# Kernel optimization log

Measured on AMD Instinct MI355X. Metric: run time of the kernel, lower is better.

## Reference

```python
import jax, jax.numpy as jnp
import numpy as np

N, E = 50000, 800000
IN_DIM, OUT_DIM, REL_DIM = 128, 64, 32
NEG_SLOPE = 0.01  # torch F.leaky_relu default


def setup_inputs() -> dict:
    key = jax.random.key(0)
    ks = jax.random.split(key, 12)
    return {
        "h": jax.random.normal(ks[0], (N, IN_DIM), jnp.float32),
        "relation": jax.random.normal(ks[1], (E, REL_DIM), jnp.float32),
        "score": jax.random.normal(ks[2], (E, 1), jnp.float32),
        "timestamp": jax.random.normal(ks[3], (E, 1), jnp.float32),
        "src": jax.random.randint(ks[4], (E,), 0, N, jnp.int32),
        "dst": jax.random.randint(ks[5], (E,), 0, N, jnp.int32),
        "W_n": jax.random.normal(ks[6], (IN_DIM, OUT_DIM), jnp.float32) / np.sqrt(IN_DIM),
        "W_r": jax.random.normal(ks[7], (REL_DIM, OUT_DIM), jnp.float32) / np.sqrt(REL_DIM),
        "W_s": jax.random.normal(ks[8], (1, OUT_DIM), jnp.float32),
        "W_t": jax.random.normal(ks[9], (1, OUT_DIM), jnp.float32),
        "a": jax.random.normal(ks[10], (5 * OUT_DIM,), jnp.float32) / np.sqrt(5 * OUT_DIM),
    }


def reference(h, relation, score, timestamp, src, dst, W_n, W_r, W_s, W_t, a):
    D = W_n.shape[1]
    z = h @ W_n                     # (N, D)
    er = relation @ W_r             # (E, D)
    es = score @ W_s                # (E, D)
    et = timestamp @ W_t            # (E, D)
    z_src = z[src]                  # (E, D) gather
    z_dst = z[dst]                  # (E, D) gather
    # attn_fc on concat([z_src, z_dst, er, es, et]) == sum of slice dot-products
    a1, a2, a3, a4, a5 = (a[0:D], a[D:2*D], a[2*D:3*D], a[3*D:4*D], a[4*D:5*D])
    logit = z_src @ a1 + z_dst @ a2 + er @ a3 + es @ a4 + et @ a5  # (E,)
    logit = jnp.where(logit >= 0, logit, NEG_SLOPE * logit)        # leaky_relu
    # segment softmax over edges grouped by dst node
    n = z.shape[0]
    seg_max = jax.ops.segment_max(logit, dst, num_segments=n)     # (N,)
    ex = jnp.exp(logit - seg_max[dst])                             # (E,)
    seg_sum = jax.ops.segment_sum(ex, dst, num_segments=n)        # (N,)
    alpha = ex / seg_sum[dst]                                      # (E,)
    # weighted scatter-sum of source features to dst nodes
    h_out = jax.ops.segment_sum(alpha[:, None] * z_src, dst, num_segments=n)  # (N, D)
    return h_out
```

## Files before the change

kernel.cpp:

```cpp
#include <hip/hip_runtime.h>

#define IN_DIM 128
#define OUT_DIM 64
#define REL_DIM 32
#define NEG_SLOPE 0.01f
#define CAP 64

__global__ __launch_bounds__(256) void k_node(const float* __restrict__ h,
                                              const float* __restrict__ W_n,
                                              const float* __restrict__ a,
                                              float* __restrict__ z,
                                              float* __restrict__ s1,
                                              float* __restrict__ s2,
                                              int* __restrict__ cnt, int n) {
    __shared__ float hs[IN_DIM * 65];
    __shared__ float Wl[64 * OUT_DIM];
    __shared__ float s1p[4][64], s2p[4][64];
    int base = blockIdx.x * 64;

    int gi = blockIdx.x * 256 + threadIdx.x;
    if (gi < n) cnt[gi] = 0;

    for (int i = threadIdx.x; i < 64 * 32; i += 256) {
        int r = i >> 5;
        int c4 = i & 31;
        float4 v = make_float4(0.f, 0.f, 0.f, 0.f);
        if (base + r < n) v = ((const float4*)(h + (size_t)(base + r) * IN_DIM))[c4];
        int k0 = c4 * 4;
        hs[(k0 + 0) * 65 + r] = v.x;
        hs[(k0 + 1) * 65 + r] = v.y;
        hs[(k0 + 2) * 65 + r] = v.z;
        hs[(k0 + 3) * 65 + r] = v.w;
    }

    int lane = threadIdx.x & 63;
    int w = __builtin_amdgcn_readfirstlane(threadIdx.x >> 6);
    int c0 = w * 16;
    int row = base + lane;

    float acc[16];
    #pragma unroll
    for (int j = 0; j < 16; ++j) acc[j] = 0.f;

    for (int kh = 0; kh < 2; ++kh) {
        __syncthreads();
        for (int i = threadIdx.x; i < 64 * OUT_DIM / 4; i += 256)
            ((float4*)Wl)[i] = ((const float4*)(W_n + (size_t)kh * 64 * OUT_DIM))[i];
        __syncthreads();
        #pragma unroll 4
        for (int kk = 0; kk < 64; ++kk) {
            float hv = hs[(kh * 64 + kk) * 65 + lane];
            const float4* Wk = (const float4*)(Wl + kk * OUT_DIM + c0);
            float4 w0 = Wk[0], w1 = Wk[1], w2 = Wk[2], w3 = Wk[3];
            acc[0]  = fmaf(hv, w0.x, acc[0]);
            acc[1]  = fmaf(hv, w0.y, acc[1]);
            acc[2]  = fmaf(hv, w0.z, acc[2]);
            acc[3]  = fmaf(hv, w0.w, acc[3]);
            acc[4]  = fmaf(hv, w1.x, acc[4]);
            acc[5]  = fmaf(hv, w1.y, acc[5]);
            acc[6]  = fmaf(hv, w1.z, acc[6]);
            acc[7]  = fmaf(hv, w1.w, acc[7]);
            acc[8]  = fmaf(hv, w2.x, acc[8]);
            acc[9]  = fmaf(hv, w2.y, acc[9]);
            acc[10] = fmaf(hv, w2.z, acc[10]);
            acc[11] = fmaf(hv, w2.w, acc[11]);
            acc[12] = fmaf(hv, w3.x, acc[12]);
            acc[13] = fmaf(hv, w3.y, acc[13]);
            acc[14] = fmaf(hv, w3.z, acc[14]);
            acc[15] = fmaf(hv, w3.w, acc[15]);
        }
    }

    float p1 = 0.f, p2 = 0.f;
    #pragma unroll
    for (int j = 0; j < 16; ++j) {
        p1 = fmaf(acc[j], a[c0 + j], p1);
        p2 = fmaf(acc[j], a[OUT_DIM + c0 + j], p2);
    }
    s1p[w][lane] = p1;
    s2p[w][lane] = p2;

    if (row < n) {
        float4* zp = (float4*)(z + (size_t)row * OUT_DIM + c0);
        zp[0] = make_float4(acc[0], acc[1], acc[2], acc[3]);
        zp[1] = make_float4(acc[4], acc[5], acc[6], acc[7]);
        zp[2] = make_float4(acc[8], acc[9], acc[10], acc[11]);
        zp[3] = make_float4(acc[12], acc[13], acc[14], acc[15]);
    }
    __syncthreads();
    if (threadIdx.x < 64 && base + (int)threadIdx.x < n) {
        int l = threadIdx.x;
        s1[base + l] = s1p[0][l] + s1p[1][l] + s1p[2][l] + s1p[3][l];
        s2[base + l] = s2p[0][l] + s2p[1][l] + s2p[2][l] + s2p[3][l];
    }
}

__global__ __launch_bounds__(256) void k_fill(const float* __restrict__ rel,
                                              const float* __restrict__ score,
                                              const float* __restrict__ ts,
                                              const int* __restrict__ src,
                                              const int* __restrict__ dst,
                                              const float* __restrict__ s1,
                                              const float* __restrict__ s2,
                                              const float* __restrict__ W_r,
                                              const float* __restrict__ W_s,
                                              const float* __restrict__ W_t,
                                              const float* __restrict__ a,
                                              int* __restrict__ cnt,
                                              int2* __restrict__ pedge, int E) {
    __shared__ __align__(16) float cw[36];
    int t = threadIdx.x;
    if (t < REL_DIM) {
        const float* a3 = a + 2 * OUT_DIM;
        float acc = 0.f;
        #pragma unroll
        for (int d2 = 0; d2 < OUT_DIM; ++d2)
            acc = fmaf(W_r[t * OUT_DIM + d2], a3[d2], acc);
        cw[t] = acc;
    } else if (t == 32) {
        float acc = 0.f;
        for (int d2 = 0; d2 < OUT_DIM; ++d2) acc = fmaf(W_s[d2], a[3 * OUT_DIM + d2], acc);
        cw[32] = acc;
    } else if (t == 33) {
        float acc = 0.f;
        for (int d2 = 0; d2 < OUT_DIM; ++d2) acc = fmaf(W_t[d2], a[4 * OUT_DIM + d2], acc);
        cw[33] = acc;
    }
    __syncthreads();

    int tid = blockIdx.x * 256 + t;
    int e = tid >> 3;
    int sub = tid & 7;
    if (e >= E) return;

    float4 w4 = ((const float4*)cw)[sub];
    float4 v = ((const float4*)rel)[(size_t)e * 8 + sub];
    float dot = v.x * w4.x + v.y * w4.y + v.z * w4.z + v.w * w4.w;
    dot += __shfl_xor(dot, 1, 8);
    dot += __shfl_xor(dot, 2, 8);
    dot += __shfl_xor(dot, 4, 8);

    if (sub == 0) {
        int s = src[e], d = dst[e];
        float lg = dot + s1[s] + s2[d] + score[e] * cw[32] + ts[e] * cw[33];
        lg = (lg >= 0.f) ? lg : NEG_SLOPE * lg;
        int rank = atomicAdd(cnt + d, 1);
        if (rank < CAP)
            pedge[((size_t)d << 6) + rank] = make_int2(s, __float_as_int(lg));
    }
}

__global__ __launch_bounds__(256) void k_out(const int* __restrict__ cnt,
                                             const int2* __restrict__ pedge,
                                             const float* __restrict__ z,
                                             float* __restrict__ out, int n) {
    int lane = threadIdx.x & 63;
    int wave = (blockIdx.x * blockDim.x + threadIdx.x) >> 6;
    int nwaves = (gridDim.x * blockDim.x) >> 6;
    int eg = lane >> 4;
    int dl = lane & 15;
    int npairs = (n + 1) >> 1;
    for (int p = wave; p < npairs; p += nwaves) {
        int nA = p * 2, nB = p * 2 + 1;
        int degA = min(cnt[nA], CAP);
        int degB = (nB < n) ? min(cnt[nB], CAP) : 0;
        int2 peA = make_int2(0, (int)0xff800000u);
        int2 peB = make_int2(0, (int)0xff800000u);
        if (lane < degA) peA = pedge[((size_t)nA << 6) + lane];
        if (lane < degB) peB = pedge[((size_t)nB << 6) + lane];
        float vA = __int_as_float(peA.y), vB = __int_as_float(peB.y);
        float mA = vA, mB = vB;
        #pragma unroll
        for (int o = 32; o > 0; o >>= 1) {
            mA = fmaxf(mA, __shfl_xor(mA, o, 64));
            mB = fmaxf(mB, __shfl_xor(mB, o, 64));
        }
        float exA = __expf(vA - mA);
        float exB = __expf(vB - mB);
        float sA = exA, sB = exB;
        #pragma unroll
        for (int o = 32; o > 0; o >>= 1) {
            sA += __shfl_xor(sA, o, 64);
            sB += __shfl_xor(sB, o, 64);
        }
        float alA = exA * (1.0f / sA);
        float alB = exB * (1.0f / sB);
        float4 accA = make_float4(0.f, 0.f, 0.f, 0.f);
        float4 accB = make_float4(0.f, 0.f, 0.f, 0.f);
        int jmax = max(degA, degB);
        for (int j0 = 0; j0 < jmax; j0 += 4) {
            int j = j0 + eg;
            int jc = (j < 64) ? j : 63;
            float wA = __shfl(alA, jc, 64);
            int  sjA = __shfl(peA.x, jc, 64);
            float wB = __shfl(alB, jc, 64);
            int  sjB = __shfl(peB.x, jc, 64);
            if (j < degA) {
                float4 zv = ((const float4*)(z + (size_t)sjA * OUT_DIM))[dl];
                accA.x = fmaf(wA, zv.x, accA.x);
                accA.y = fmaf(wA, zv.y, accA.y);
                accA.z = fmaf(wA, zv.z, accA.z);
                accA.w = fmaf(wA, zv.w, accA.w);
            }
            if (j < degB) {
                float4 zv = ((const float4*)(z + (size_t)sjB * OUT_DIM))[dl];
                accB.x = fmaf(wB, zv.x, accB.x);
                accB.y = fmaf(wB, zv.y, accB.y);
                accB.z = fmaf(wB, zv.z, accB.z);
                accB.w = fmaf(wB, zv.w, accB.w);
            }
        }
        #pragma unroll
        for (int o = 16; o <= 32; o <<= 1) {
            accA.x += __shfl_xor(accA.x, o, 64);
            accA.y += __shfl_xor(accA.y, o, 64);
            accA.z += __shfl_xor(accA.z, o, 64);
            accA.w += __shfl_xor(accA.w, o, 64);
            accB.x += __shfl_xor(accB.x, o, 64);
            accB.y += __shfl_xor(accB.y, o, 64);
            accB.z += __shfl_xor(accB.z, o, 64);
            accB.w += __shfl_xor(accB.w, o, 64);
        }
        if (eg == 0) {
            ((float4*)(out + (size_t)nA * OUT_DIM))[dl] = accA;
        } else if (eg == 1 && nB < n) {
            ((float4*)(out + (size_t)nB * OUT_DIM))[dl] = accB;
        }
    }
}

extern "C" void kernel_launch(void* const* d_in, const int* in_sizes, int n_in,
                              void* d_out, int out_size, void* d_ws, size_t ws_size,
                              hipStream_t stream) {
    const float* h         = (const float*)d_in[0];
    const float* relation  = (const float*)d_in[1];
    const float* score     = (const float*)d_in[2];
    const float* timestamp = (const float*)d_in[3];
    const int*   src       = (const int*)d_in[4];
    const int*   dst       = (const int*)d_in[5];
    const float* W_n       = (const float*)d_in[6];
    const float* W_r       = (const float*)d_in[7];
    const float* W_s       = (const float*)d_in[8];
    const float* W_t       = (const float*)d_in[9];
    const float* a         = (const float*)d_in[10];

    int n = in_sizes[0] / IN_DIM;
    int E = in_sizes[4];

    float* ws   = (float*)d_ws;
    float* z    = ws;
    float* s1   = z + (size_t)n * OUT_DIM;
    float* s2   = s1 + n;
    int*   cnt  = (int*)(s2 + n);
    int2*  pedge = (int2*)(cnt + n);

    float* out = (float*)d_out;

    k_node<<<(n + 63) / 64, 256, 0, stream>>>(h, W_n, a, z, s1, s2, cnt, n);

    int nfb = (int)(((long long)E * 8 + 255) / 256);
    k_fill<<<nfb, 256, 0, stream>>>(relation, score, timestamp, src, dst,
                                    s1, s2, W_r, W_s, W_t, a, cnt, pedge, E);

    int npairs = (n + 1) >> 1;
    k_out<<<(npairs + 3) / 4, 256, 0, stream>>>(cnt, pedge, z, out, n);
}
```

Measured before the change: 312.6 us.

## Store node features in fp16 and bucket edge indices instead of packed pairs

Node projections z are written as fp16 so the per-edge gather in the aggregation kernel moves half the bytes, converting back to fp32 before accumulation. The attention constant vector is computed once in the node kernel instead of in every fill block. The per-destination bucket now stores edge ids, with logits written to a separate array, so the output kernel performs extra indirect loads of logit and src. This trades precision of z and additional random 4-byte gathers for lower gather bandwidth.

```diff
diff --git a/kernel.cpp b/kernel.cpp
--- a/kernel.cpp
+++ b/kernel.cpp
@@ -1,4 +1,5 @@
 #include <hip/hip_runtime.h>
+#include <hip/hip_fp16.h>
 
 #define IN_DIM 128
 #define OUT_DIM 64
@@ -8,10 +9,14 @@
 
 __global__ __launch_bounds__(256) void k_node(const float* __restrict__ h,
                                               const float* __restrict__ W_n,
+                                              const float* __restrict__ W_r,
+                                              const float* __restrict__ W_s,
+                                              const float* __restrict__ W_t,
                                               const float* __restrict__ a,
-                                              float* __restrict__ z,
+                                              __half* __restrict__ zh,
                                               float* __restrict__ s1,
                                               float* __restrict__ s2,
+                                              float* __restrict__ consts,
                                               int* __restrict__ cnt, int n) {
     __shared__ float hs[IN_DIM * 65];
     __shared__ float Wl[64 * OUT_DIM];
@@ -20,6 +25,28 @@
 
     int gi = blockIdx.x * 256 + threadIdx.x;
     if (gi < n) cnt[gi] = 0;
+
+    if (blockIdx.x == 0) {
+        int t = threadIdx.x;
+        if (t < REL_DIM) {
+            const float* a3 = a + 2 * OUT_DIM;
+            float acc = 0.f;
+            #pragma unroll
+            for (int d2 = 0; d2 < OUT_DIM; ++d2)
+                acc = fmaf(W_r[t * OUT_DIM + d2], a3[d2], acc);
+            consts[t] = acc;
+        } else if (t == 32) {
+            float acc = 0.f;
+            for (int d2 = 0; d2 < OUT_DIM; ++d2) acc = fmaf(W_s[d2], a[3 * OUT_DIM + d2], acc);
+            consts[32] = acc;
+        } else if (t == 33) {
+            float acc = 0.f;
+            for (int d2 = 0; d2 < OUT_DIM; ++d2) acc = fmaf(W_t[d2], a[4 * OUT_DIM + d2], acc);
+            consts[33] = acc;
+        } else if (t == 34 || t == 35) {
+            consts[t] = 0.f;
+        }
+    }
 
     for (int i = threadIdx.x; i < 64 * 32; i += 256) {
         int r = i >> 5;
@@ -81,11 +108,10 @@
     s2p[w][lane] = p2;
 
     if (row < n) {
-        float4* zp = (float4*)(z + (size_t)row * OUT_DIM + c0);
-        zp[0] = make_float4(acc[0], acc[1], acc[2], acc[3]);
-        zp[1] = make_float4(acc[4], acc[5], acc[6], acc[7]);
-        zp[2] = make_float4(acc[8], acc[9], acc[10], acc[11]);
-        zp[3] = make_float4(acc[12], acc[13], acc[14], acc[15]);
+        __half2* zp = (__half2*)(zh + (size_t)row * OUT_DIM + c0);
+        #pragma unroll
+        for (int j = 0; j < 8; ++j)
+            zp[j] = __floats2half2_rn(acc[2 * j], acc[2 * j + 1]);
     }
     __syncthreads();
     if (threadIdx.x < 64 && base + (int)threadIdx.x < n) {
@@ -102,30 +128,13 @@
                                               const int* __restrict__ dst,
                                               const float* __restrict__ s1,
                                               const float* __restrict__ s2,
-                                              const float* __restrict__ W_r,
-                                              const float* __restrict__ W_s,
-                                              const float* __restrict__ W_t,
-                                              const float* __restrict__ a,
+                                              const float* __restrict__ consts,
                                               int* __restrict__ cnt,
-                                              int2* __restrict__ pedge, int E) {
+                                              int* __restrict__ pidx,
+                                              float* __restrict__ llog, int E) {
     __shared__ __align__(16) float cw[36];
     int t = threadIdx.x;
-    if (t < REL_DIM) {
-        const float* a3 = a + 2 * OUT_DIM;
-        float acc = 0.f;
-        #pragma unroll
-        for (int d2 = 0; d2 < OUT_DIM; ++d2)
-            acc = fmaf(W_r[t * OUT_DIM + d2], a3[d2], acc);
-        cw[t] = acc;
-    } else if (t == 32) {
-        float acc = 0.f;
-        for (int d2 = 0; d2 < OUT_DIM; ++d2) acc = fmaf(W_s[d2], a[3 * OUT_DIM + d2], acc);
-        cw[32] = acc;
-    } else if (t == 33) {
-        float acc = 0.f;
-        for (int d2 = 0; d2 < OUT_DIM; ++d2) acc = fmaf(W_t[d2], a[4 * OUT_DIM + d2], acc);
-        cw[33] = acc;
-    }
+    if (t < 36) cw[t] = consts[t];
     __syncthreads();
 
     int tid = blockIdx.x * 256 + t;
@@ -144,15 +153,18 @@
         int s = src[e], d = dst[e];
         float lg = dot + s1[s] + s2[d] + score[e] * cw[32] + ts[e] * cw[33];
         lg = (lg >= 0.f) ? lg : NEG_SLOPE * lg;
+        llog[e] = lg;
         int rank = atomicAdd(cnt + d, 1);
         if (rank < CAP)
-            pedge[((size_t)d << 6) + rank] = make_int2(s, __float_as_int(lg));
+            pidx[((size_t)d << 6) + rank] = e;
     }
 }
 
 __global__ __launch_bounds__(256) void k_out(const int* __restrict__ cnt,
-                                             const int2* __restrict__ pedge,
-                                             const float* __restrict__ z,
+                                             const int* __restrict__ pidx,
+                                             const float* __restrict__ llog,
+                                             const int* __restrict__ src,
+                                             const __half* __restrict__ zh,
                                              float* __restrict__ out, int n) {
     int lane = threadIdx.x & 63;
     int wave = (blockIdx.x * blockDim.x + threadIdx.x) >> 6;
@@ -164,11 +176,12 @@
         int nA = p * 2, nB = p * 2 + 1;
         int degA = min(cnt[nA], CAP);
         int degB = (nB < n) ? min(cnt[nB], CAP) : 0;
-        int2 peA = make_int2(0, (int)0xff800000u);
-        int2 peB = make_int2(0, (int)0xff800000u);
-        if (lane < degA) peA = pedge[((size_t)nA << 6) + lane];
-        if (lane < degB) peB = pedge[((size_t)nB << 6) + lane];
-        float vA = __int_as_float(peA.y), vB = __int_as_float(peB.y);
+        int eA = (lane < degA) ? pidx[((size_t)nA << 6) + lane] : -1;
+        int eB = (lane < degB) ? pidx[((size_t)nB << 6) + lane] : -1;
+        float vA = (eA >= 0) ? llog[eA] : __int_as_float(0xff800000u);
+        float vB = (eB >= 0) ? llog[eB] : __int_as_float(0xff800000u);
+        int srcA = (eA >= 0) ? src[eA] : 0;
+        int srcB = (eB >= 0) ? src[eB] : 0;
         float mA = vA, mB = vB;
         #pragma unroll
         for (int o = 32; o > 0; o >>= 1) {
@@ -177,14 +190,14 @@
         }
         float exA = __expf(vA - mA);
         float exB = __expf(vB - mB);
-        float sA = exA, sB = exB;
+        float sumA = exA, sumB = exB;
         #pragma unroll
         for (int o = 32; o > 0; o >>= 1) {
-            sA += __shfl_xor(sA, o, 64);
-            sB += __shfl_xor(sB, o, 64);
-        }
-        float alA = exA * (1.0f / sA);
-        float alB = exB * (1.0f / sB);
+            sumA += __shfl_xor(sumA, o, 64);
+            sumB += __shfl_xor(sumB, o, 64);
+        }
+        float alA = exA * (1.0f / sumA);
+        float alB = exB * (1.0f / sumB);
         float4 accA = make_float4(0.f, 0.f, 0.f, 0.f);
         float4 accB = make_float4(0.f, 0.f, 0.f, 0.f);
         int jmax = max(degA, degB);
@@ -192,22 +205,26 @@
             int j = j0 + eg;
             int jc = (j < 64) ? j : 63;
             float wA = __shfl(alA, jc, 64);
-            int  sjA = __shfl(peA.x, jc, 64);
+            int  sjA = __shfl(srcA, jc, 64);
             float wB = __shfl(alB, jc, 64);
-            int  sjB = __shfl(peB.x, jc, 64);
+            int  sjB = __shfl(srcB, jc, 64);
             if (j < degA) {
-                float4 zv = ((const float4*)(z + (size_t)sjA * OUT_DIM))[dl];
-                accA.x = fmaf(wA, zv.x, accA.x);
-                accA.y = fmaf(wA, zv.y, accA.y);
-                accA.z = fmaf(wA, zv.z, accA.z);
-                accA.w = fmaf(wA, zv.w, accA.w);
+                uint2 u = ((const uint2*)(zh + (size_t)sjA * OUT_DIM))[dl];
+                float2 f01 = __half22float2(*(const __half2*)&u.x);
+                float2 f23 = __half22float2(*(const __half2*)&u.y);
+                accA.x = fmaf(wA, f01.x, accA.x);
+                accA.y = fmaf(wA, f01.y, accA.y);
+                accA.z = fmaf(wA, f23.x, accA.z);
+                accA.w = fmaf(wA, f23.y, accA.w);
             }
             if (j < degB) {
-                float4 zv = ((const float4*)(z + (size_t)sjB * OUT_DIM))[dl];
-                accB.x = fmaf(wB, zv.x, accB.x);
-                accB.y = fmaf(wB, zv.y, accB.y);
-                accB.z = fmaf(wB, zv.z, accB.z);
-                accB.w = fmaf(wB, zv.w, accB.w);
+                uint2 u = ((const uint2*)(zh + (size_t)sjB * OUT_DIM))[dl];
+                float2 f01 = __half22float2(*(const __half2*)&u.x);
+                float2 f23 = __half22float2(*(const __half2*)&u.y);
+                accB.x = fmaf(wB, f01.x, accB.x);
+                accB.y = fmaf(wB, f01.y, accB.y);
+                accB.z = fmaf(wB, f23.x, accB.z);
+                accB.w = fmaf(wB, f23.y, accB.w);
             }
         }
         #pragma unroll
@@ -247,21 +264,23 @@
     int n = in_sizes[0] / IN_DIM;
     int E = in_sizes[4];
 
-    float* ws   = (float*)d_ws;
-    float* z    = ws;
-    float* s1   = z + (size_t)n * OUT_DIM;
-    float* s2   = s1 + n;
-    int*   cnt  = (int*)(s2 + n);
-    int2*  pedge = (int2*)(cnt + n);
+    __half* zh    = (__half*)d_ws;
+    float*  s1    = (float*)(zh + (size_t)n * OUT_DIM);
+    float*  s2    = s1 + n;
+    float*  consts = s2 + n;
+    int*    cnt   = (int*)(consts + 64);
+    float*  llog  = (float*)(cnt + n);
+    int*    pidx  = (int*)(llog + E);
 
     float* out = (float*)d_out;
 
-    k_node<<<(n + 63) / 64, 256, 0, stream>>>(h, W_n, a, z, s1, s2, cnt, n);
+    k_node<<<(n + 63) / 64, 256, 0, stream>>>(h, W_n, W_r, W_s, W_t, a,
+                                              zh, s1, s2, consts, cnt, n);
 
     int nfb = (int)(((long long)E * 8 + 255) / 256);
     k_fill<<<nfb, 256, 0, stream>>>(relation, score, timestamp, src, dst,
-                                    s1, s2, W_r, W_s, W_t, a, cnt, pedge, E);
+                                    s1, s2, consts, cnt, pidx, llog, E);
 
     int npairs = (n + 1) >> 1;
-    k_out<<<(npairs + 3) / 4, 256, 0, stream>>>(cnt, pedge, z, out, n);
-}
+    k_out<<<(npairs + 3) / 4, 256, 0, stream>>>(cnt, pidx, llog, src, zh, out, n);
+}
```

New measurement: 285.9 us. -8.5%, faster.
